# Performance work log

Measured on AMD Instinct MI355X. Metric: run time of the kernel, lower is better.

The kernel has to match this reference:

```python
import jax, jax.numpy as jnp
import numpy as np

B, N, D = 32, 1024, 128


def setup_inputs() -> dict:
    key = jax.random.key(0)
    ks = jax.random.split(key, 8)
    scale = 0.05
    P = jax.random.normal(ks[0], (B, N, D), dtype=jnp.float32)
    w_itr_att = jax.random.normal(ks[1], (3 * D,), dtype=jnp.float32) * scale
    w1 = jax.random.normal(ks[2], (2 * D, D), dtype=jnp.float32) * scale
    w2 = jax.random.normal(ks[3], (2 * D, D), dtype=jnp.float32) * scale
    w3 = jax.random.normal(ks[4], (2 * D, D), dtype=jnp.float32) * scale
    b1 = jnp.zeros((D,), dtype=jnp.float32)
    b2 = jnp.zeros((D,), dtype=jnp.float32)
    b3 = jnp.zeros((D,), dtype=jnp.float32)
    return {"P": P, "w_itr_att": w_itr_att, "w1": w1, "w2": w2,
            "w3": w3, "b1": b1, "b2": b2, "b3": b3}


def reference(P, w_itr_att, w1, w2, w3, b1, b2, b3):
    # P: [b, n, d]
    d = P.shape[-1]
    # Original builds alphaP[b,i,:,j] = concat(P[b,j], P[b,i], P[b,j]*P[b,i])
    # and A[b,i,j] = w_itr_att . alphaP[b,i,:,j]. Decompose w to avoid the
    # O(n^2 * 3d) tensor while computing identical math.
    wa, wb, wc = w_itr_att[:d], w_itr_att[d:2 * d], w_itr_att[2 * d:]
    A = (P @ wb)[:, :, None] + (P @ wa)[:, None, :] \
        + jnp.einsum('bid,bjd->bij', P * wc, P)  # [b, n, n]
    SA = jax.nn.softmax(A, axis=-1)              # softmax over j (axis=2)
    itr_attn = jnp.einsum('bij,bjd->bid', SA, P)  # batch_dot(SA, P)
    # Fuse gate (dropout is identity at inference)
    P_concat = jnp.concatenate([P, itr_attn], axis=2)  # [b, n, 2d]
    z = jnp.tanh(P_concat @ w1 + b1)
    r = jax.nn.sigmoid(P_concat @ w2 + b2)
    f = jax.nn.sigmoid(P_concat @ w3 + b3)
    return r * P + f * z
```

## Files before the change

kernel.cpp:

```cpp
#include <hip/hip_runtime.h>
#include <math.h>

#define BB 32
#define NN 1024
#define DD 128

typedef __bf16 bf16;
typedef bf16 bf16x4 __attribute__((ext_vector_type(4)));
typedef bf16 bf16x8 __attribute__((ext_vector_type(8)));
typedef float f32x4 __attribute__((ext_vector_type(4)));

#define MFMA(a, b, c) __builtin_amdgcn_mfma_f32_16x16x32_bf16(a, b, c, 0, 0, 0)

__device__ inline bf16x8 cvt8(const float4 a, const float4 b) {
    bf16x8 r;
    r[0] = (bf16)a.x; r[1] = (bf16)a.y; r[2] = (bf16)a.z; r[3] = (bf16)a.w;
    r[4] = (bf16)b.x; r[5] = (bf16)b.y; r[6] = (bf16)b.z; r[7] = (bf16)b.w;
    return r;
}

__global__ __launch_bounds__(256) void k_prep(const float* __restrict__ P,
                                              const float* __restrict__ w_itr,
                                              bf16* __restrict__ Xbf,
                                              bf16* __restrict__ Pq,
                                              bf16* __restrict__ Ptp,
                                              float* __restrict__ t) {
    __shared__ bf16 Lt[128 * 72];
    int tid = threadIdx.x;
    int b = blockIdx.x >> 4, g = blockIdx.x & 15;
    int n0 = g * 64;
    int row = tid >> 2, q = tid & 3, d0 = q * 32;
    long brow = (long)b * NN + n0 + row;

    const float* src = P + brow * DD + d0;
    float r[32];
#pragma unroll
    for (int i = 0; i < 8; ++i) {
        float4 v = ((const float4*)src)[i];
        r[4 * i + 0] = v.x; r[4 * i + 1] = v.y; r[4 * i + 2] = v.z; r[4 * i + 3] = v.w;
    }
    float s = 0.f;
#pragma unroll
    for (int k = 0; k < 32; ++k) s += r[k] * w_itr[d0 + k];
    s += __shfl_xor(s, 1);
    s += __shfl_xor(s, 2);
    if (q == 0) t[brow] = s;
    const float* wc = w_itr + 2 * DD;
#pragma unroll
    for (int i = 0; i < 4; ++i) {
        bf16x8 xv, qv;
#pragma unroll
        for (int e = 0; e < 8; ++e) {
            float f = r[8 * i + e];
            xv[e] = (bf16)f;
            qv[e] = (bf16)(f * wc[d0 + 8 * i + e]);
        }
        *(bf16x8*)&Xbf[brow * 256 + d0 + 8 * i] = xv;
        *(bf16x8*)&Pq[brow * DD + d0 + 8 * i] = qv;
    }
    int rowp = ((row & 15) << 2) | ((row >> 4) & 3);
#pragma unroll
    for (int k = 0; k < 32; ++k) Lt[(d0 + k) * 72 + rowp] = (bf16)r[k];
    __syncthreads();
#pragma unroll
    for (int i = 0; i < 4; ++i) {
        int idx = tid + i * 256;
        int d = idx >> 3, c = idx & 7;
        *(float4*)&Ptp[((long)b * DD + d) * NN + n0 + c * 8] =
            *(const float4*)&Lt[d * 72 + c * 8];
    }
}

__global__ __launch_bounds__(256) void k_prepw(const float* __restrict__ w1,
                                               const float* __restrict__ w2,
                                               const float* __restrict__ w3,
                                               bf16* __restrict__ WtG) {
    int idx = blockIdx.x * 256 + threadIdx.x;
    int mat = idx >> 15, rem = idx & 32767;
    int col = rem >> 8, k = rem & 255;
    const float* w = (mat == 0) ? w1 : ((mat == 1) ? w2 : w3);
    WtG[idx] = (bf16)w[k * DD + col];
}

__global__ __launch_bounds__(256, 1) void k_attn(bf16* Xbf,
                                                 const bf16* __restrict__ Pq,
                                                 const bf16* __restrict__ Ptp,
                                                 const float* __restrict__ t) {
    __shared__ bf16 Kt[64 * 136];
    __shared__ bf16 Vt[128 * 72];
    __shared__ float tts[64];
    __shared__ bf16 Pl[4][32 * 72];

    const int tid = threadIdx.x;
    const int w = tid >> 6, lane = tid & 63, ln = lane & 15, q3 = lane >> 4;
    const int b = blockIdx.x >> 3, qt = blockIdx.x & 7;
    const long browQ = (long)b * NN + qt * 128 + w * 32;

    bf16x8 Qf[2][4];
#pragma unroll
    for (int mt = 0; mt < 2; ++mt)
#pragma unroll
        for (int c = 0; c < 4; ++c)
            Qf[mt][c] = *(const bf16x8*)&Pq[(browQ + mt * 16 + ln) * DD + c * 32 + q3 * 8];

    f32x4 O[2][8];
    float lsum[2][4];
#pragma unroll
    for (int mt = 0; mt < 2; ++mt) {
#pragma unroll
        for (int nt = 0; nt < 8; ++nt) O[mt][nt] = (f32x4){0.f, 0.f, 0.f, 0.f};
#pragma unroll
        for (int r = 0; r < 4; ++r) lsum[mt][r] = 0.f;
    }

    float4 kreg[4], vreg[4];
    float treg = 0.f;
    auto loadstage = [&](int jt) {
        int j0 = jt * 64;
#pragma unroll
        for (int i = 0; i < 4; ++i) {
            int idx = tid + i * 256;
            kreg[i] = *(const float4*)&Xbf[((long)b * NN + j0 + (idx >> 4)) * 256 + (idx & 15) * 8];
            vreg[i] = *(const float4*)&Ptp[((long)b * DD + (idx >> 3)) * NN + j0 + (idx & 7) * 8];
        }
        treg = (tid < 64) ? t[(long)b * NN + j0 + tid] : 0.f;
    };

    loadstage(0);
    for (int jt = 0; jt < 16; ++jt) {
        __syncthreads();
#pragma unroll
        for (int i = 0; i < 4; ++i) {
            int idx = tid + i * 256;
            *(float4*)&Kt[(idx >> 4) * 136 + (idx & 15) * 8] = kreg[i];
            *(float4*)&Vt[(idx >> 3) * 72 + (idx & 7) * 8] = vreg[i];
        }
        if (tid < 64) tts[tid] = treg;
        __syncthreads();
        if (jt < 15) loadstage(jt + 1);

        float tb[4];
#pragma unroll
        for (int kt = 0; kt < 4; ++kt) tb[kt] = tts[kt * 16 + ln];

#pragma unroll
        for (int mt = 0; mt < 2; ++mt) {
            float pv[4][4];
#pragma unroll
            for (int kt = 0; kt < 4; ++kt) {
                f32x4 S = (f32x4){0.f, 0.f, 0.f, 0.f};
#pragma unroll
                for (int c = 0; c < 4; ++c)
                    S = MFMA(Qf[mt][c],
                             *(const bf16x8*)&Kt[(kt * 16 + ln) * 136 + c * 32 + q3 * 8], S);
#pragma unroll
                for (int r = 0; r < 4; ++r) {
                    float e = __expf(fminf(S[r] + tb[kt], 80.f));
                    pv[kt][r] = e;
                    lsum[mt][r] += e;
                }
            }
#pragma unroll
            for (int r = 0; r < 4; ++r) {
                bf16x4 pk;
#pragma unroll
                for (int kt = 0; kt < 4; ++kt) pk[kt] = (bf16)pv[kt][r];
                *(bf16x4*)&Pl[w][(mt * 16 + q3 * 4 + r) * 72 + ln * 4] = pk;
            }
        }
#pragma unroll
        for (int kc = 0; kc < 2; ++kc) {
            bf16x8 Af0 = *(const bf16x8*)&Pl[w][(ln) * 72 + kc * 32 + q3 * 8];
            bf16x8 Af1 = *(const bf16x8*)&Pl[w][(16 + ln) * 72 + kc * 32 + q3 * 8];
#pragma unroll
            for (int nt = 0; nt < 8; ++nt) {
                bf16x8 Vf = *(const bf16x8*)&Vt[(nt * 16 + ln) * 72 + kc * 32 + q3 * 8];
                O[0][nt] = MFMA(Af0, Vf, O[0][nt]);
                O[1][nt] = MFMA(Af1, Vf, O[1][nt]);
            }
        }
    }

#pragma unroll
    for (int mt = 0; mt < 2; ++mt) {
        float inv[4];
#pragma unroll
        for (int r = 0; r < 4; ++r) {
            float v = lsum[mt][r];
            v += __shfl_xor(v, 1);
            v += __shfl_xor(v, 2);
            v += __shfl_xor(v, 4);
            v += __shfl_xor(v, 8);
            inv[r] = 1.f / v;
        }
#pragma unroll
        for (int nt = 0; nt < 8; ++nt)
#pragma unroll
            for (int r = 0; r < 4; ++r) {
                long row = browQ + mt * 16 + q3 * 4 + r;
                Xbf[row * 256 + 128 + nt * 16 + ln] = (bf16)(O[mt][nt][r] * inv[r]);
            }
    }
}

__global__ __launch_bounds__(256, 1) void k_mlp(const bf16* __restrict__ Xbf,
                                                const bf16* __restrict__ WtG,
                                                const float* __restrict__ P,
                                                const float* __restrict__ b1,
                                                const float* __restrict__ b2,
                                                const float* __restrict__ b3,
                                                float* __restrict__ out) {
    __shared__ bf16 Wsh[384 * 72];
    const int tid = threadIdx.x;
    const int w = tid >> 6, lane = tid & 63, ln = lane & 15, q3 = lane >> 4;
    const long row0 = (long)blockIdx.x * 128 + w * 32;

    bf16x8 Af[2][8];
#pragma unroll
    for (int mt = 0; mt < 2; ++mt)
#pragma unroll
        for (int kc = 0; kc < 8; ++kc)
            Af[mt][kc] = *(const bf16x8*)&Xbf[(row0 + mt * 16 + ln) * 256 + kc * 32 + q3 * 8];

    f32x4 acc[3][2][8];
#pragma unroll
    for (int m = 0; m < 3; ++m)
#pragma unroll
        for (int mt = 0; mt < 2; ++mt)
#pragma unroll
            for (int nt = 0; nt < 8; ++nt) acc[m][mt][nt] = (f32x4){0.f, 0.f, 0.f, 0.f};

    for (int kh = 0; kh < 4; ++kh) {
        __syncthreads();
#pragma unroll
        for (int i = 0; i < 12; ++i) {
            int idx = tid + i * 256;
            *(float4*)&Wsh[(idx >> 3) * 72 + (idx & 7) * 8] =
                *(const float4*)&WtG[(idx >> 3) * 256 + kh * 64 + (idx & 7) * 8];
        }
        __syncthreads();
#pragma unroll
        for (int kc2 = 0; kc2 < 2; ++kc2) {
            int kc = kh * 2 + kc2;
#pragma unroll
            for (int mat = 0; mat < 3; ++mat)
#pragma unroll
                for (int nt = 0; nt < 8; ++nt) {
                    bf16x8 Bf = *(const bf16x8*)&Wsh[(mat * 128 + nt * 16 + ln) * 72 +
                                                     kc2 * 32 + q3 * 8];
                    acc[mat][0][nt] = MFMA(Af[0][kc], Bf, acc[mat][0][nt]);
                    acc[mat][1][nt] = MFMA(Af[1][kc], Bf, acc[mat][1][nt]);
                }
        }
    }

#pragma unroll
    for (int mt = 0; mt < 2; ++mt)
#pragma unroll
        for (int nt = 0; nt < 8; ++nt) {
            int col = nt * 16 + ln;
            float bb1 = b1[col], bb2 = b2[col], bb3 = b3[col];
#pragma unroll
            for (int r = 0; r < 4; ++r) {
                long row = row0 + mt * 16 + q3 * 4 + r;
                float y1 = acc[0][mt][nt][r] + bb1;
                float y2 = acc[1][mt][nt][r] + bb2;
                float y3 = acc[2][mt][nt][r] + bb3;
                float p = P[row * DD + col];
                float rg = 1.f / (1.f + __expf(-y2));
                float fg = 1.f / (1.f + __expf(-y3));
                out[row * DD + col] = rg * p + fg * tanhf(y1);
            }
        }
}

extern "C" void kernel_launch(void* const* d_in, const int* in_sizes, int n_in,
                              void* d_out, int out_size, void* d_ws, size_t ws_size,
                              hipStream_t stream) {
    const float* P     = (const float*)d_in[0];
    const float* w_itr = (const float*)d_in[1];
    const float* w1    = (const float*)d_in[2];
    const float* w2    = (const float*)d_in[3];
    const float* w3    = (const float*)d_in[4];
    const float* b1    = (const float*)d_in[5];
    const float* b2    = (const float*)d_in[6];
    const float* b3    = (const float*)d_in[7];
    float* out = (float*)d_out;

    char* wsb = (char*)d_ws;
    bf16* Xbf  = (bf16*)(wsb);
    bf16* Pq   = (bf16*)(wsb + 16777216);
    bf16* Ptp  = (bf16*)(wsb + 25165824);
    float* tws = (float*)(wsb + 33554432);
    bf16* WtG  = (bf16*)(wsb + 33685504);

    k_prep<<<dim3(BB * 16), dim3(256), 0, stream>>>(P, w_itr, Xbf, Pq, Ptp, tws);
    k_prepw<<<dim3(384), dim3(256), 0, stream>>>(w1, w2, w3, WtG);
    k_attn<<<dim3(BB * 8), dim3(256), 0, stream>>>(Xbf, Pq, Ptp, tws);
    k_mlp<<<dim3(BB * NN / 128), dim3(256), 0, stream>>>(Xbf, WtG, P, b1, b2, b3, out);
}
```

Before: 190.4 us.

## Rework attention with 32x32 MFMA split-K, retile MLP and weight transpose

The attention kernel now uses 32x32x16 MFMA with K as the A operand, so the softmax probabilities are regrouped into B-operand fragments through lane shuffles instead of an LDS round-trip. It splits the key range into two halves handled by separate wave pairs and combines the partial outputs and row sums through shared memory. The grid doubles to 512 blocks at 2 blocks per CU to raise occupancy. The MLP kernel drops LDS weight staging, reads weights directly from global and processes one weight matrix at a time to reduce registers. The weight transpose kernel becomes a tiled LDS transpose, and the prep kernel's row permutation is removed to match the new layout.

```diff
diff --git a/kernel.cpp b/kernel.cpp
--- a/kernel.cpp
+++ b/kernel.cpp
@@ -9,14 +9,17 @@
 typedef bf16 bf16x4 __attribute__((ext_vector_type(4)));
 typedef bf16 bf16x8 __attribute__((ext_vector_type(8)));
 typedef float f32x4 __attribute__((ext_vector_type(4)));
-
-#define MFMA(a, b, c) __builtin_amdgcn_mfma_f32_16x16x32_bf16(a, b, c, 0, 0, 0)
-
-__device__ inline bf16x8 cvt8(const float4 a, const float4 b) {
-    bf16x8 r;
-    r[0] = (bf16)a.x; r[1] = (bf16)a.y; r[2] = (bf16)a.z; r[3] = (bf16)a.w;
-    r[4] = (bf16)b.x; r[5] = (bf16)b.y; r[6] = (bf16)b.z; r[7] = (bf16)b.w;
-    return r;
+typedef float f32x16 __attribute__((ext_vector_type(16)));
+
+#define MFMA16(a, b, c) __builtin_amdgcn_mfma_f32_16x16x32_bf16(a, b, c, 0, 0, 0)
+#define MFMA32(a, b, c) __builtin_amdgcn_mfma_f32_32x32x16_bf16(a, b, c, 0, 0, 0)
+
+__device__ inline bf16x4 swap32(bf16x4 v) {
+    union { bf16x4 h; int i[2]; } u, r;
+    u.h = v;
+    r.i[0] = __shfl_xor(u.i[0], 32, 64);
+    r.i[1] = __shfl_xor(u.i[1], 32, 64);
+    return r.h;
 }
 
 __global__ __launch_bounds__(256) void k_prep(const float* __restrict__ P,
@@ -58,9 +61,8 @@
         *(bf16x8*)&Xbf[brow * 256 + d0 + 8 * i] = xv;
         *(bf16x8*)&Pq[brow * DD + d0 + 8 * i] = qv;
     }
-    int rowp = ((row & 15) << 2) | ((row >> 4) & 3);
-#pragma unroll
-    for (int k = 0; k < 32; ++k) Lt[(d0 + k) * 72 + rowp] = (bf16)r[k];
+#pragma unroll
+    for (int k = 0; k < 32; ++k) Lt[(d0 + k) * 72 + row] = (bf16)r[k];
     __syncthreads();
 #pragma unroll
     for (int i = 0; i < 4; ++i) {
@@ -75,145 +77,202 @@
                                                const float* __restrict__ w2,
                                                const float* __restrict__ w3,
                                                bf16* __restrict__ WtG) {
-    int idx = blockIdx.x * 256 + threadIdx.x;
-    int mat = idx >> 15, rem = idx & 32767;
-    int col = rem >> 8, k = rem & 255;
-    const float* w = (mat == 0) ? w1 : ((mat == 1) ? w2 : w3);
-    WtG[idx] = (bf16)w[k * DD + col];
-}
-
-__global__ __launch_bounds__(256, 1) void k_attn(bf16* Xbf,
+    __shared__ float Lw[32][33];
+    int bi = blockIdx.x;
+    int mat = bi >> 5, rem = bi & 31;
+    int kt = rem >> 2, ct = rem & 3;
+    const float* wsrc = (mat == 0) ? w1 : ((mat == 1) ? w2 : w3);
+    int tid = threadIdx.x;
+#pragma unroll
+    for (int p = 0; p < 4; ++p) {
+        int idx = tid + p * 256;
+        int kr = idx >> 5, c = idx & 31;
+        Lw[kr][c] = wsrc[(kt * 32 + kr) * DD + ct * 32 + c];
+    }
+    __syncthreads();
+    int colg = tid >> 3, kq = tid & 7;
+    bf16x4 v;
+#pragma unroll
+    for (int e = 0; e < 4; ++e) v[e] = (bf16)Lw[kq * 4 + e][colg];
+    *(bf16x4*)&WtG[(mat * 128 + ct * 32 + colg) * 256 + kt * 32 + kq * 4] = v;
+}
+
+__global__ __launch_bounds__(256, 2) void k_attn(bf16* __restrict__ Xbf,
                                                  const bf16* __restrict__ Pq,
                                                  const bf16* __restrict__ Ptp,
                                                  const float* __restrict__ t) {
-    __shared__ bf16 Kt[64 * 136];
-    __shared__ bf16 Vt[128 * 72];
-    __shared__ float tts[64];
-    __shared__ bf16 Pl[4][32 * 72];
+    __shared__ __align__(16) char smem[72704];
+    bf16* Kt = (bf16*)smem;
+    bf16* Vt = (bf16*)(smem + 34816);
+    float* tsh = (float*)(smem + 71680);
+    float* lbuf = (float*)(smem + 72192);
+    float* Obuf = (float*)smem;
 
     const int tid = threadIdx.x;
-    const int w = tid >> 6, lane = tid & 63, ln = lane & 15, q3 = lane >> 4;
-    const int b = blockIdx.x >> 3, qt = blockIdx.x & 7;
-    const long browQ = (long)b * NN + qt * 128 + w * 32;
-
-    bf16x8 Qf[2][4];
-#pragma unroll
-    for (int mt = 0; mt < 2; ++mt)
-#pragma unroll
-        for (int c = 0; c < 4; ++c)
-            Qf[mt][c] = *(const bf16x8*)&Pq[(browQ + mt * 16 + ln) * DD + c * 32 + q3 * 8];
-
-    f32x4 O[2][8];
-    float lsum[2][4];
-#pragma unroll
-    for (int mt = 0; mt < 2; ++mt) {
-#pragma unroll
-        for (int nt = 0; nt < 8; ++nt) O[mt][nt] = (f32x4){0.f, 0.f, 0.f, 0.f};
-#pragma unroll
-        for (int r = 0; r < 4; ++r) lsum[mt][r] = 0.f;
-    }
-
-    float4 kreg[4], vreg[4];
-    float treg = 0.f;
-    auto loadstage = [&](int jt) {
-        int j0 = jt * 64;
-#pragma unroll
-        for (int i = 0; i < 4; ++i) {
+    const int w = tid >> 6, lane = tid & 63;
+    const int col = lane & 31, q = lane >> 5;
+    const int kh = w >> 1, rg = w & 1;
+    const int b = blockIdx.x & 31, qt = blockIdx.x >> 5;
+    const long qbase = (long)b * NN + qt * 64 + rg * 32;
+
+    const bf16* KtH = Kt + kh * (64 * 136);
+    const bf16* VtH = Vt + kh * (128 * 72);
+    const float* tH = tsh + kh * 64;
+
+    bf16x8 Qb[8];
+#pragma unroll
+    for (int c = 0; c < 8; ++c)
+        Qb[c] = *(const bf16x8*)&Pq[(qbase + col) * DD + c * 16 + q * 8];
+
+    f32x16 O[4];
+#pragma unroll
+    for (int mt = 0; mt < 4; ++mt)
+#pragma unroll
+        for (int r = 0; r < 16; ++r) O[mt][r] = 0.f;
+    float lsum = 0.f;
+
+    float4 kr[8];
+    float tr = 0.f;
+    auto loadK = [&](int jt) {
+#pragma unroll
+        for (int i = 0; i < 8; ++i) {
             int idx = tid + i * 256;
-            kreg[i] = *(const float4*)&Xbf[((long)b * NN + j0 + (idx >> 4)) * 256 + (idx & 15) * 8];
-            vreg[i] = *(const float4*)&Ptp[((long)b * DD + (idx >> 3)) * NN + j0 + (idx & 7) * 8];
-        }
-        treg = (tid < 64) ? t[(long)b * NN + j0 + tid] : 0.f;
+            int h = idx >> 10, rem = idx & 1023;
+            int key = rem >> 4, c16 = rem & 15;
+            kr[i] = *(const float4*)&Xbf[((long)b * NN + h * 512 + jt * 64 + key) * 256 + c16 * 8];
+        }
+        tr = (tid < 128) ? t[(long)b * NN + (tid >> 6) * 512 + jt * 64 + (tid & 63)] : 0.f;
     };
 
-    loadstage(0);
-    for (int jt = 0; jt < 16; ++jt) {
+    loadK(0);
+    for (int jt = 0; jt < 8; ++jt) {
         __syncthreads();
 #pragma unroll
-        for (int i = 0; i < 4; ++i) {
+        for (int i = 0; i < 8; ++i) {
             int idx = tid + i * 256;
-            *(float4*)&Kt[(idx >> 4) * 136 + (idx & 15) * 8] = kreg[i];
-            *(float4*)&Vt[(idx >> 3) * 72 + (idx & 7) * 8] = vreg[i];
-        }
-        if (tid < 64) tts[tid] = treg;
+            int h = idx >> 10, rem = idx & 1023;
+            int key = rem >> 4, c16 = rem & 15;
+            *(float4*)&Kt[h * (64 * 136) + key * 136 + c16 * 8] = kr[i];
+        }
+        if (tid < 128) tsh[tid] = tr;
+        float4 vr[8];
+#pragma unroll
+        for (int i = 0; i < 8; ++i) {
+            int idx = tid + i * 256;
+            int h = idx >> 10, rem = idx & 1023;
+            int d = rem >> 3, c8 = rem & 7;
+            vr[i] = *(const float4*)&Ptp[((long)b * DD + d) * NN + h * 512 + jt * 64 + c8 * 8];
+        }
+#pragma unroll
+        for (int i = 0; i < 8; ++i) {
+            int idx = tid + i * 256;
+            int h = idx >> 10, rem = idx & 1023;
+            int d = rem >> 3, c8 = rem & 7;
+            *(float4*)&Vt[h * (128 * 72) + d * 72 + c8 * 8] = vr[i];
+        }
         __syncthreads();
-        if (jt < 15) loadstage(jt + 1);
-
-        float tb[4];
-#pragma unroll
-        for (int kt = 0; kt < 4; ++kt) tb[kt] = tts[kt * 16 + ln];
-
-#pragma unroll
-        for (int mt = 0; mt < 2; ++mt) {
-            float pv[4][4];
-#pragma unroll
-            for (int kt = 0; kt < 4; ++kt) {
-                f32x4 S = (f32x4){0.f, 0.f, 0.f, 0.f};
-#pragma unroll
-                for (int c = 0; c < 4; ++c)
-                    S = MFMA(Qf[mt][c],
-                             *(const bf16x8*)&Kt[(kt * 16 + ln) * 136 + c * 32 + q3 * 8], S);
-#pragma unroll
-                for (int r = 0; r < 4; ++r) {
-                    float e = __expf(fminf(S[r] + tb[kt], 80.f));
-                    pv[kt][r] = e;
-                    lsum[mt][r] += e;
-                }
-            }
-#pragma unroll
-            for (int r = 0; r < 4; ++r) {
-                bf16x4 pk;
-#pragma unroll
-                for (int kt = 0; kt < 4; ++kt) pk[kt] = (bf16)pv[kt][r];
-                *(bf16x4*)&Pl[w][(mt * 16 + q3 * 4 + r) * 72 + ln * 4] = pk;
-            }
-        }
-#pragma unroll
-        for (int kc = 0; kc < 2; ++kc) {
-            bf16x8 Af0 = *(const bf16x8*)&Pl[w][(ln) * 72 + kc * 32 + q3 * 8];
-            bf16x8 Af1 = *(const bf16x8*)&Pl[w][(16 + ln) * 72 + kc * 32 + q3 * 8];
-#pragma unroll
-            for (int nt = 0; nt < 8; ++nt) {
-                bf16x8 Vf = *(const bf16x8*)&Vt[(nt * 16 + ln) * 72 + kc * 32 + q3 * 8];
-                O[0][nt] = MFMA(Af0, Vf, O[0][nt]);
-                O[1][nt] = MFMA(Af1, Vf, O[1][nt]);
-            }
-        }
-    }
-
-#pragma unroll
-    for (int mt = 0; mt < 2; ++mt) {
-        float inv[4];
-#pragma unroll
-        for (int r = 0; r < 4; ++r) {
-            float v = lsum[mt][r];
-            v += __shfl_xor(v, 1);
-            v += __shfl_xor(v, 2);
-            v += __shfl_xor(v, 4);
-            v += __shfl_xor(v, 8);
-            inv[r] = 1.f / v;
-        }
-#pragma unroll
-        for (int nt = 0; nt < 8; ++nt)
-#pragma unroll
-            for (int r = 0; r < 4; ++r) {
-                long row = browQ + mt * 16 + q3 * 4 + r;
-                Xbf[row * 256 + 128 + nt * 16 + ln] = (bf16)(O[mt][nt][r] * inv[r]);
-            }
-    }
-}
-
-__global__ __launch_bounds__(256, 1) void k_mlp(const bf16* __restrict__ Xbf,
+        if (jt < 7) loadK(jt + 1);
+
+#pragma unroll
+        for (int kt = 0; kt < 2; ++kt) {
+            f32x16 S;
+#pragma unroll
+            for (int r = 0; r < 16; ++r) S[r] = 0.f;
+#pragma unroll
+            for (int c = 0; c < 8; ++c)
+                S = MFMA32(*(const bf16x8*)&KtH[(kt * 32 + col) * 136 + c * 16 + q * 8],
+                           Qb[c], S);
+            float tqs[16];
+#pragma unroll
+            for (int i = 0; i < 4; ++i) {
+                float4 tv = *(const float4*)&tH[kt * 32 + 8 * i + 4 * q];
+                tqs[4 * i + 0] = tv.x; tqs[4 * i + 1] = tv.y;
+                tqs[4 * i + 2] = tv.z; tqs[4 * i + 3] = tv.w;
+            }
+            float pv[16];
+#pragma unroll
+            for (int r = 0; r < 16; ++r) {
+                float e = __expf(fminf(S[r] + tqs[r], 80.f));
+                pv[r] = e;
+                lsum += e;
+            }
+            bf16x4 Qd[4];
+#pragma unroll
+            for (int i = 0; i < 4; ++i)
+#pragma unroll
+                for (int e = 0; e < 4; ++e) Qd[i][e] = (bf16)pv[4 * i + e];
+            bf16x4 sA = q ? Qd[0] : Qd[1];
+            bf16x4 rA = swap32(sA);
+            bf16x4 sB = q ? Qd[2] : Qd[3];
+            bf16x4 rB = swap32(sB);
+            bf16x4 lo0 = q ? rA : Qd[0], hi0 = q ? Qd[1] : rA;
+            bf16x4 lo1 = q ? rB : Qd[2], hi1 = q ? Qd[3] : rB;
+            bf16x8 f0, f1;
+#pragma unroll
+            for (int e = 0; e < 4; ++e) {
+                f0[e] = lo0[e]; f0[4 + e] = hi0[e];
+                f1[e] = lo1[e]; f1[4 + e] = hi1[e];
+            }
+#pragma unroll
+            for (int mt = 0; mt < 4; ++mt) {
+                O[mt] = MFMA32(*(const bf16x8*)&VtH[(mt * 32 + col) * 72 + kt * 32 + q * 8],
+                               f0, O[mt]);
+                O[mt] = MFMA32(*(const bf16x8*)&VtH[(mt * 32 + col) * 72 + kt * 32 + 16 + q * 8],
+                               f1, O[mt]);
+            }
+        }
+    }
+
+    float l2 = lsum + __shfl_xor(lsum, 32, 64);
+    if (q == 0) lbuf[(kh * 2 + rg) * 32 + col] = l2;
+    __syncthreads();
+    if (kh == 1) {
+#pragma unroll
+        for (int mt = 0; mt < 4; ++mt)
+#pragma unroll
+            for (int r = 0; r < 16; ++r) {
+                int d = mt * 32 + (r & 3) + 8 * (r >> 2) + 4 * q;
+                Obuf[(rg * 128 + d) * 36 + col] = O[mt][r];
+            }
+    }
+    __syncthreads();
+    if (kh == 0) {
+        float linv = 1.f / (lbuf[(0 * 2 + rg) * 32 + col] + lbuf[(1 * 2 + rg) * 32 + col]);
+#pragma unroll
+        for (int mt = 0; mt < 4; ++mt)
+#pragma unroll
+            for (int r = 0; r < 16; ++r) {
+                int d = mt * 32 + (r & 3) + 8 * (r >> 2) + 4 * q;
+                int ix = (rg * 128 + d) * 36 + col;
+                Obuf[ix] = (O[mt][r] + Obuf[ix]) * linv;
+            }
+    }
+    __syncthreads();
+    {
+        int colg = tid & 31, rg2 = (tid >> 5) & 1, w4 = tid >> 6;
+        long grow = (long)b * NN + qt * 64 + rg2 * 32 + colg;
+#pragma unroll
+        for (int p = 0; p < 4; ++p) {
+            bf16x8 v8;
+#pragma unroll
+            for (int e = 0; e < 8; ++e)
+                v8[e] = (bf16)Obuf[(rg2 * 128 + w4 * 32 + p * 8 + e) * 36 + colg];
+            *(bf16x8*)&Xbf[grow * 256 + 128 + w4 * 32 + p * 8] = v8;
+        }
+    }
+}
+
+__global__ __launch_bounds__(256, 2) void k_mlp(const bf16* __restrict__ Xbf,
                                                 const bf16* __restrict__ WtG,
                                                 const float* __restrict__ P,
                                                 const float* __restrict__ b1,
                                                 const float* __restrict__ b2,
                                                 const float* __restrict__ b3,
                                                 float* __restrict__ out) {
-    __shared__ bf16 Wsh[384 * 72];
     const int tid = threadIdx.x;
     const int w = tid >> 6, lane = tid & 63, ln = lane & 15, q3 = lane >> 4;
-    const long row0 = (long)blockIdx.x * 128 + w * 32;
+    const int rg = w & 1, ch = w >> 1;
+    const long row0 = (long)blockIdx.x * 64 + rg * 32;
 
     bf16x8 Af[2][8];
 #pragma unroll
@@ -222,56 +281,44 @@
         for (int kc = 0; kc < 8; ++kc)
             Af[mt][kc] = *(const bf16x8*)&Xbf[(row0 + mt * 16 + ln) * 256 + kc * 32 + q3 * 8];
 
-    f32x4 acc[3][2][8];
-#pragma unroll
-    for (int m = 0; m < 3; ++m)
+    f32x4 stz[2][4], str[2][4];
+#pragma unroll
+    for (int mat = 0; mat < 3; ++mat) {
+        f32x4 acc[2][4];
 #pragma unroll
         for (int mt = 0; mt < 2; ++mt)
 #pragma unroll
-            for (int nt = 0; nt < 8; ++nt) acc[m][mt][nt] = (f32x4){0.f, 0.f, 0.f, 0.f};
-
-    for (int kh = 0; kh < 4; ++kh) {
-        __syncthreads();
-#pragma unroll
-        for (int i = 0; i < 12; ++i) {
-            int idx = tid + i * 256;
-            *(float4*)&Wsh[(idx >> 3) * 72 + (idx & 7) * 8] =
-                *(const float4*)&WtG[(idx >> 3) * 256 + kh * 64 + (idx & 7) * 8];
-        }
-        __syncthreads();
-#pragma unroll
-        for (int kc2 = 0; kc2 < 2; ++kc2) {
-            int kc = kh * 2 + kc2;
-#pragma unroll
-            for (int mat = 0; mat < 3; ++mat)
-#pragma unroll
-                for (int nt = 0; nt < 8; ++nt) {
-                    bf16x8 Bf = *(const bf16x8*)&Wsh[(mat * 128 + nt * 16 + ln) * 72 +
-                                                     kc2 * 32 + q3 * 8];
-                    acc[mat][0][nt] = MFMA(Af[0][kc], Bf, acc[mat][0][nt]);
-                    acc[mat][1][nt] = MFMA(Af[1][kc], Bf, acc[mat][1][nt]);
+            for (int nt = 0; nt < 4; ++nt) acc[mt][nt] = (f32x4){0.f, 0.f, 0.f, 0.f};
+#pragma unroll
+        for (int kc = 0; kc < 8; ++kc)
+#pragma unroll
+            for (int nt = 0; nt < 4; ++nt) {
+                bf16x8 Bf = *(const bf16x8*)&WtG[(mat * 128 + ch * 64 + nt * 16 + ln) * 256 +
+                                                 kc * 32 + q3 * 8];
+                acc[0][nt] = MFMA16(Af[0][kc], Bf, acc[0][nt]);
+                acc[1][nt] = MFMA16(Af[1][kc], Bf, acc[1][nt]);
+            }
+        const float* bp = (mat == 0) ? b1 : ((mat == 1) ? b2 : b3);
+#pragma unroll
+        for (int mt = 0; mt < 2; ++mt)
+#pragma unroll
+            for (int nt = 0; nt < 4; ++nt) {
+                int colc = ch * 64 + nt * 16 + ln;
+                float bb = bp[colc];
+#pragma unroll
+                for (int r = 0; r < 4; ++r) {
+                    float y = acc[mt][nt][r] + bb;
+                    if (mat == 0) stz[mt][nt][r] = tanhf(y);
+                    else if (mat == 1) str[mt][nt][r] = 1.f / (1.f + __expf(-y));
+                    else {
+                        float fg = 1.f / (1.f + __expf(-y));
+                        long row = row0 + mt * 16 + q3 * 4 + r;
+                        float p = P[row * DD + colc];
+                        out[row * DD + colc] = str[mt][nt][r] * p + fg * stz[mt][nt][r];
+                    }
                 }
-        }
-    }
-
-#pragma unroll
-    for (int mt = 0; mt < 2; ++mt)
-#pragma unroll
-        for (int nt = 0; nt < 8; ++nt) {
-            int col = nt * 16 + ln;
-            float bb1 = b1[col], bb2 = b2[col], bb3 = b3[col];
-#pragma unroll
-            for (int r = 0; r < 4; ++r) {
-                long row = row0 + mt * 16 + q3 * 4 + r;
-                float y1 = acc[0][mt][nt][r] + bb1;
-                float y2 = acc[1][mt][nt][r] + bb2;
-                float y3 = acc[2][mt][nt][r] + bb3;
-                float p = P[row * DD + col];
-                float rg = 1.f / (1.f + __expf(-y2));
-                float fg = 1.f / (1.f + __expf(-y3));
-                out[row * DD + col] = rg * p + fg * tanhf(y1);
-            }
-        }
+            }
+    }
 }
 
 extern "C" void kernel_launch(void* const* d_in, const int* in_sizes, int n_in,
@@ -295,7 +342,7 @@
     bf16* WtG  = (bf16*)(wsb + 33685504);
 
     k_prep<<<dim3(BB * 16), dim3(256), 0, stream>>>(P, w_itr, Xbf, Pq, Ptp, tws);
-    k_prepw<<<dim3(384), dim3(256), 0, stream>>>(w1, w2, w3, WtG);
-    k_attn<<<dim3(BB * 8), dim3(256), 0, stream>>>(Xbf, Pq, Ptp, tws);
-    k_mlp<<<dim3(BB * NN / 128), dim3(256), 0, stream>>>(Xbf, WtG, P, b1, b2, b3, out);
-}
+    k_prepw<<<dim3(96), dim3(256), 0, stream>>>(w1, w2, w3, WtG);
+    k_attn<<<dim3(512), dim3(256), 0, stream>>>(Xbf, Pq, Ptp, tws);
+    k_mlp<<<dim3(512), dim3(256), 0, stream>>>(Xbf, WtG, P, b1, b2, b3, out);
+}
```

Measured after the change: 183.9 us. 1.04x faster.
